# Kernel tuning notes

Measured on AMD Instinct MI355X. Metric: run time of the kernel, lower is better.

Reference implementation:

```python
import jax, jax.numpy as jnp
import numpy as np


def _grid_sample_3d(src, grid):
    """Trilinear grid_sample, align_corners=True, zero padding.
    src: [B,C,D,H,W], grid: [B,D,H,W,3] with last dim (x,y,z) ~ (W,H,D) in [-1,1].
    """
    B, C, D, H, W = src.shape
    gx, gy, gz = grid[..., 0], grid[..., 1], grid[..., 2]
    # unnormalize (align_corners=True): -1 -> 0, +1 -> dim-1
    ix = (gx + 1.0) * ((W - 1) / 2.0)
    iy = (gy + 1.0) * ((H - 1) / 2.0)
    iz = (gz + 1.0) * ((D - 1) / 2.0)
    ix0 = jnp.floor(ix); iy0 = jnp.floor(iy); iz0 = jnp.floor(iz)
    fx = ix - ix0; fy = iy - iy0; fz = iz - iz0  # fractional parts
    x0 = ix0.astype(jnp.int32); y0 = iy0.astype(jnp.int32); z0 = iz0.astype(jnp.int32)

    src_flat = src.reshape(B, C, D * H * W)
    out = jnp.zeros((B, C, D * H * W), dtype=src.dtype)
    for dz in (0, 1):
        for dy in (0, 1):
            for dx in (0, 1):
                xc = x0 + dx; yc = y0 + dy; zc = z0 + dz
                w = ((fx if dx else 1.0 - fx)
                     * (fy if dy else 1.0 - fy)
                     * (fz if dz else 1.0 - fz))
                valid = ((xc >= 0) & (xc < W) & (yc >= 0) & (yc < H)
                         & (zc >= 0) & (zc < D))
                xs = jnp.clip(xc, 0, W - 1)
                ys = jnp.clip(yc, 0, H - 1)
                zs = jnp.clip(zc, 0, D - 1)
                lin = ((zs * H + ys) * W + xs).reshape(B, -1)  # [B, DHW]
                vals = jax.vmap(lambda s, i: jnp.take(s, i, axis=1))(src_flat, lin)  # [B,C,DHW]
                out = out + (w * valid).reshape(B, 1, -1).astype(src.dtype) * vals
    return out.reshape(B, C, D, H, W)


def _affine_grid_3d(theta, D, H, W):
    """torch affine_grid (align_corners=True) for size [B,3,D,H,W]. Returns [B,D,H,W,3]."""
    xs = jnp.linspace(-1.0, 1.0, W, dtype=theta.dtype)
    ys = jnp.linspace(-1.0, 1.0, H, dtype=theta.dtype)
    zs = jnp.linspace(-1.0, 1.0, D, dtype=theta.dtype)
    bx = jnp.broadcast_to(xs[None, None, :], (D, H, W))
    by = jnp.broadcast_to(ys[None, :, None], (D, H, W))
    bz = jnp.broadcast_to(zs[:, None, None], (D, H, W))
    base = jnp.stack([bx, by, bz, jnp.ones((D, H, W), theta.dtype)], axis=-1)  # [D,H,W,4]
    return jnp.einsum('bij,dhwj->bdhwi', theta, base)


def setup_inputs() -> dict:
    key = jax.random.key(0)
    k1, k2 = jax.random.split(key)
    B, C, D, H, W = 2, 2, 160, 192, 224
    src = jax.random.normal(k1, (B, C, D, H, W), dtype=jnp.float32)
    eye = jnp.concatenate([jnp.eye(3, dtype=jnp.float32),
                           jnp.zeros((3, 1), jnp.float32)], axis=1)  # [3,4]
    mat = eye[None] + 0.05 * jax.random.normal(k2, (B, 3, 4), dtype=jnp.float32)
    return {"src": src, "mat": mat}


def reference(src, mat):
    B, C, D, H, W = src.shape
    norm = jnp.array([[1, 1, 1, D], [1, 1, 1, H], [1, 1, 1, W]], dtype=mat.dtype)
    theta = mat / norm[None]  # normalize translation column by spatial dims
    grid = _affine_grid_3d(theta, D, H, W)
    return _grid_sample_3d(src, grid)
```

## Files before the change

kernel.cpp:

```cpp
#include <hip/hip_runtime.h>

#define BB 2
#define CC 2
#define DD 160
#define HH 192
#define WW 224
#define DHW (DD * HH * WW)

typedef float f2v __attribute__((ext_vector_type(2)));

__device__ __forceinline__ f2v load2u(const float* p) {
    struct __attribute__((packed)) S { f2v v; };
    return ((const S*)p)->v;
}

__global__ __launch_bounds__(256) void affine_sample_kernel(
    const float* __restrict__ src,
    const float* __restrict__ mat,
    float* __restrict__ out)
{
    int idx = blockIdx.x * blockDim.x + threadIdx.x;
    if (idx >= DHW) return;
    int b = blockIdx.y;

    int w = idx % WW;
    int t = idx / WW;
    int h = t % HH;
    int d = t / HH;

    const float* m = mat + b * 12;
    float a00 = m[0], a01 = m[1], a02 = m[2],  a03 = m[3]  * (1.0f / (float)DD);
    float a10 = m[4], a11 = m[5], a12 = m[6],  a13 = m[7]  * (1.0f / (float)HH);
    float a20 = m[8], a21 = m[9], a22 = m[10], a23 = m[11] * (1.0f / (float)WW);

    float xn = -1.0f + (float)w * (2.0f / (float)(WW - 1));
    float yn = -1.0f + (float)h * (2.0f / (float)(HH - 1));
    float zn = -1.0f + (float)d * (2.0f / (float)(DD - 1));

    float gx = a00 * xn + a01 * yn + a02 * zn + a03;
    float gy = a10 * xn + a11 * yn + a12 * zn + a13;
    float gz = a20 * xn + a21 * yn + a22 * zn + a23;

    float ix = (gx + 1.0f) * ((float)(WW - 1) * 0.5f);
    float iy = (gy + 1.0f) * ((float)(HH - 1) * 0.5f);
    float iz = (gz + 1.0f) * ((float)(DD - 1) * 0.5f);

    float fx0 = floorf(ix), fy0 = floorf(iy), fz0 = floorf(iz);
    float fx = ix - fx0, fy = iy - fy0, fz = iz - fz0;
    int x0 = (int)fx0, y0 = (int)fy0, z0 = (int)fz0;
    int x1 = x0 + 1, y1 = y0 + 1, z1 = z0 + 1;

    float wx0 = (x0 >= 0 && x0 < WW) ? (1.0f - fx) : 0.0f;
    float wx1 = (x1 >= 0 && x1 < WW) ? fx          : 0.0f;
    float wy0 = (y0 >= 0 && y0 < HH) ? (1.0f - fy) : 0.0f;
    float wy1 = (y1 >= 0 && y1 < HH) ? fy          : 0.0f;
    float wz0 = (z0 >= 0 && z0 < DD) ? (1.0f - fz) : 0.0f;
    float wz1 = (z1 >= 0 && z1 < DD) ? fz          : 0.0f;

    int xc0 = min(max(x0, 0), WW - 1), xc1 = min(max(x1, 0), WW - 1);
    int yc0 = min(max(y0, 0), HH - 1), yc1 = min(max(y1, 0), HH - 1);
    int zc0 = min(max(z0, 0), DD - 1), zc1 = min(max(z1, 0), DD - 1);

    int xb   = min(xc0, WW - 2);
    int sel0 = xc0 - xb;
    int sel1 = xc1 - xb;

    const float* s0 = src + (size_t)b * CC * DHW + xb;
    const float* s1 = s0 + DHW;

    int r00 = (zc0 * HH + yc0) * WW;
    int r01 = (zc0 * HH + yc1) * WW;
    int r10 = (zc1 * HH + yc0) * WW;
    int r11 = (zc1 * HH + yc1) * WW;

    f2v pa00 = load2u(s0 + r00);
    f2v pa01 = load2u(s0 + r01);
    f2v pa10 = load2u(s0 + r10);
    f2v pa11 = load2u(s0 + r11);
    f2v pb00 = load2u(s1 + r00);
    f2v pb01 = load2u(s1 + r01);
    f2v pb10 = load2u(s1 + r10);
    f2v pb11 = load2u(s1 + r11);

    float w00 = wz0 * wy0, w01 = wz0 * wy1;
    float w10 = wz1 * wy0, w11 = wz1 * wy1;

    #define ROWVAL(p) (wx0 * (sel0 ? (p)[1] : (p)[0]) + wx1 * (sel1 ? (p)[1] : (p)[0]))
    float acc0 = w00 * ROWVAL(pa00) + w01 * ROWVAL(pa01)
               + w10 * ROWVAL(pa10) + w11 * ROWVAL(pa11);
    float acc1 = w00 * ROWVAL(pb00) + w01 * ROWVAL(pb01)
               + w10 * ROWVAL(pb10) + w11 * ROWVAL(pb11);
    #undef ROWVAL

    float* o = out + (size_t)b * CC * DHW + idx;
    __builtin_nontemporal_store(acc0, o);
    __builtin_nontemporal_store(acc1, o + DHW);
}

extern "C" void kernel_launch(void* const* d_in, const int* in_sizes, int n_in,
                              void* d_out, int out_size, void* d_ws, size_t ws_size,
                              hipStream_t stream) {
    const float* src = (const float*)d_in[0];
    const float* mat = (const float*)d_in[1];
    float* out = (float*)d_out;

    dim3 block(256);
    dim3 grid((DHW + 255) / 256, BB);
    affine_sample_kernel<<<grid, block, 0, stream>>>(src, mat, out);
}
```

Baseline: 250.9 us.

## Swizzle block order across XCDs and fold affine coefficients into FMAs

Remaps blockIdx.x so that consecutive hardware block IDs, which are dealt round-robin across the 8 XCDs, become contiguous spatial chunks per XCD. The aim is better L2 locality for the gathered source rows. It also folds normalization and unnormalization into precomputed affine coefficients evaluated with FMAs, and replaces the per-row select logic with precomputed A/B weights in an FMA chain. The remap relies on NBLK being divisible by 8 (26880 is), and the algebraic refold can shift rounding slightly.

Result: no change. 251.0 us (+0.0%).

```diff
diff --git a/kernel.cpp b/kernel.cpp
--- a/kernel.cpp
+++ b/kernel.cpp
@@ -6,12 +6,13 @@
 #define HH 192
 #define WW 224
 #define DHW (DD * HH * WW)
+#define NBLK ((DHW + 255) / 256)
 
 typedef float f2v __attribute__((ext_vector_type(2)));
 
-__device__ __forceinline__ f2v load2u(const float* p) {
+__device__ __forceinline__ f2v load2u(const float* base, int off) {
     struct __attribute__((packed)) S { f2v v; };
-    return ((const S*)p)->v;
+    return ((const S*)(base + off))->v;
 }
 
 __global__ __launch_bounds__(256) void affine_sample_kernel(
@@ -19,7 +20,9 @@
     const float* __restrict__ mat,
     float* __restrict__ out)
 {
-    int idx = blockIdx.x * blockDim.x + threadIdx.x;
+    int bx = blockIdx.x;
+    int bs = (bx & 7) * (NBLK / 8) + (bx >> 3);
+    int idx = bs * 256 + threadIdx.x;
     if (idx >= DHW) return;
     int b = blockIdx.y;
 
@@ -33,17 +36,19 @@
     float a10 = m[4], a11 = m[5], a12 = m[6],  a13 = m[7]  * (1.0f / (float)HH);
     float a20 = m[8], a21 = m[9], a22 = m[10], a23 = m[11] * (1.0f / (float)WW);
 
-    float xn = -1.0f + (float)w * (2.0f / (float)(WW - 1));
-    float yn = -1.0f + (float)h * (2.0f / (float)(HH - 1));
-    float zn = -1.0f + (float)d * (2.0f / (float)(DD - 1));
+    const float sw = (float)(WW - 1) * 0.5f, sh = (float)(HH - 1) * 0.5f, sd = (float)(DD - 1) * 0.5f;
+    const float tw = 2.0f / (float)(WW - 1), th = 2.0f / (float)(HH - 1), td = 2.0f / (float)(DD - 1);
+    float C00 = a00 * tw * sw, C01 = a01 * th * sw, C02 = a02 * td * sw;
+    float C03 = (-(a00 + a01 + a02) + a03 + 1.0f) * sw;
+    float C10 = a10 * tw * sh, C11 = a11 * th * sh, C12 = a12 * td * sh;
+    float C13 = (-(a10 + a11 + a12) + a13 + 1.0f) * sh;
+    float C20 = a20 * tw * sd, C21 = a21 * th * sd, C22 = a22 * td * sd;
+    float C23 = (-(a20 + a21 + a22) + a23 + 1.0f) * sd;
 
-    float gx = a00 * xn + a01 * yn + a02 * zn + a03;
-    float gy = a10 * xn + a11 * yn + a12 * zn + a13;
-    float gz = a20 * xn + a21 * yn + a22 * zn + a23;
-
-    float ix = (gx + 1.0f) * ((float)(WW - 1) * 0.5f);
-    float iy = (gy + 1.0f) * ((float)(HH - 1) * 0.5f);
-    float iz = (gz + 1.0f) * ((float)(DD - 1) * 0.5f);
+    float fw = (float)w, fh = (float)h, fd = (float)d;
+    float ix = fmaf(C00, fw, fmaf(C01, fh, fmaf(C02, fd, C03)));
+    float iy = fmaf(C10, fw, fmaf(C11, fh, fmaf(C12, fd, C13)));
+    float iz = fmaf(C20, fw, fmaf(C21, fh, fmaf(C22, fd, C23)));
 
     float fx0 = floorf(ix), fy0 = floorf(iy), fz0 = floorf(iz);
     float fx = ix - fx0, fy = iy - fy0, fz = iz - fz0;
@@ -64,37 +69,46 @@
     int xb   = min(xc0, WW - 2);
     int sel0 = xc0 - xb;
     int sel1 = xc1 - xb;
+    float A = wx0 * (float)(1 - sel0) + wx1 * (float)(1 - sel1);
+    float B = wx0 * (float)sel0      + wx1 * (float)sel1;
 
-    const float* s0 = src + (size_t)b * CC * DHW + xb;
-    const float* s1 = s0 + DHW;
+    const float* sbase0 = src + (size_t)b * CC * DHW;
+    const float* sbase1 = sbase0 + DHW;
 
-    int r00 = (zc0 * HH + yc0) * WW;
-    int r01 = (zc0 * HH + yc1) * WW;
-    int r10 = (zc1 * HH + yc0) * WW;
-    int r11 = (zc1 * HH + yc1) * WW;
+    int o00 = (zc0 * HH + yc0) * WW + xb;
+    int o01 = (zc0 * HH + yc1) * WW + xb;
+    int o10 = (zc1 * HH + yc0) * WW + xb;
+    int o11 = (zc1 * HH + yc1) * WW + xb;
 
-    f2v pa00 = load2u(s0 + r00);
-    f2v pa01 = load2u(s0 + r01);
-    f2v pa10 = load2u(s0 + r10);
-    f2v pa11 = load2u(s0 + r11);
-    f2v pb00 = load2u(s1 + r00);
-    f2v pb01 = load2u(s1 + r01);
-    f2v pb10 = load2u(s1 + r10);
-    f2v pb11 = load2u(s1 + r11);
+    f2v pa00 = load2u(sbase0, o00);
+    f2v pa01 = load2u(sbase0, o01);
+    f2v pa10 = load2u(sbase0, o10);
+    f2v pa11 = load2u(sbase0, o11);
+    f2v pb00 = load2u(sbase1, o00);
+    f2v pb01 = load2u(sbase1, o01);
+    f2v pb10 = load2u(sbase1, o10);
+    f2v pb11 = load2u(sbase1, o11);
 
     float w00 = wz0 * wy0, w01 = wz0 * wy1;
     float w10 = wz1 * wy0, w11 = wz1 * wy1;
 
-    #define ROWVAL(p) (wx0 * (sel0 ? (p)[1] : (p)[0]) + wx1 * (sel1 ? (p)[1] : (p)[0]))
-    float acc0 = w00 * ROWVAL(pa00) + w01 * ROWVAL(pa01)
-               + w10 * ROWVAL(pa10) + w11 * ROWVAL(pa11);
-    float acc1 = w00 * ROWVAL(pb00) + w01 * ROWVAL(pb01)
-               + w10 * ROWVAL(pb10) + w11 * ROWVAL(pb11);
-    #undef ROWVAL
+    float a00w = w00 * A, b00w = w00 * B;
+    float a01w = w01 * A, b01w = w01 * B;
+    float a10w = w10 * A, b10w = w10 * B;
+    float a11w = w11 * A, b11w = w11 * B;
 
-    float* o = out + (size_t)b * CC * DHW + idx;
-    __builtin_nontemporal_store(acc0, o);
-    __builtin_nontemporal_store(acc1, o + DHW);
+    float acc0 = fmaf(a00w, pa00[0], fmaf(b00w, pa00[1],
+                 fmaf(a01w, pa01[0], fmaf(b01w, pa01[1],
+                 fmaf(a10w, pa10[0], fmaf(b10w, pa10[1],
+                 fmaf(a11w, pa11[0], b11w * pa11[1])))))));
+    float acc1 = fmaf(a00w, pb00[0], fmaf(b00w, pb00[1],
+                 fmaf(a01w, pb01[0], fmaf(b01w, pb01[1],
+                 fmaf(a10w, pb10[0], fmaf(b10w, pb10[1],
+                 fmaf(a11w, pb11[0], b11w * pb11[1])))))));
+
+    float* obase = out + (size_t)b * CC * DHW;
+    __builtin_nontemporal_store(acc0, obase + idx);
+    __builtin_nontemporal_store(acc1, obase + DHW + idx);
 }
 
 extern "C" void kernel_launch(void* const* d_in, const int* in_sizes, int n_in,
@@ -105,6 +119,6 @@
     float* out = (float*)d_out;
 
     dim3 block(256);
-    dim3 grid((DHW + 255) / 256, BB);
+    dim3 grid(NBLK, BB);
     affine_sample_kernel<<<grid, block, 0, stream>>>(src, mat, out);
 }
```
